# Performance work log

Hardware: AMD Instinct MI355X
Metric: run time of the kernel (lower is better)

Reference implementation:

```python
import jax, jax.numpy as jnp
import numpy as np

B, C_IN, H, W = 32, 3, 256, 256
PATCH = 16
E, C_OUT = 8, 8
C_PROJ = 16
NUM_CLASSES = 1000
SPP_LEVELS = (1, 2, 4)
GATE_STEEPNESS = 10.0


def _conv(x, w, b, pad):
    # x: [N,C,H,W], w: [O,C,kh,kw]
    y = jax.lax.conv_general_dilated(x, w, (1, 1), [(pad, pad), (pad, pad)],
                                     dimension_numbers=('NCHW', 'OIHW', 'NCHW'))
    return y + b[None, :, None, None]


def _forward(X, expert_w, expert_b, proj_w, proj_b, keys, threshold,
             final_w, final_b, lin_w, lin_b):
    Bx, C, Hx, Wx = X.shape
    h, w = Hx // PATCH, Wx // PATCH
    P = h * w
    # 1) patch extraction: [B,C,H,W] -> [B*P, C, ph, pw]
    xp = (X.reshape(Bx, C, h, PATCH, w, PATCH)
           .transpose(0, 2, 4, 1, 3, 5)
           .reshape(Bx * P, C, PATCH, PATCH))
    # 2) router: conv projection -> global avg pool -> key similarity -> softmax -> soft threshold gate
    proj = _conv(xp, proj_w, proj_b, 1)                 # [BP, 16, ph, pw]
    pooled = proj.mean(axis=(2, 3))                     # [BP, 16]
    scores = jax.nn.softmax(pooled @ keys.T, axis=-1)   # [BP, E]
    gate = scores * jax.nn.sigmoid((scores - threshold) * GATE_STEEPNESS)
    gate = gate / (gate.sum(axis=-1, keepdims=True) + 1e-9)
    gate = gate.reshape(Bx, P, E)
    # 3) all experts fused as one conv with E*C_OUT output channels (conv3x3 pad1 + ReLU)
    ew = expert_w.reshape(E * C_OUT, C, 3, 3)
    eb = expert_b.reshape(E * C_OUT)
    outs = jax.nn.relu(_conv(xp, ew, eb, 1))            # [BP, E*Cout, ph, pw]
    outs = outs.reshape(Bx, P, E, C_OUT, PATCH, PATCH)
    # 4) router-weighted combine over experts
    comb = jnp.einsum('bpe,bpeclm->bpclm', gate, outs)  # [B,P,Cout,ph,pw]
    # 5) reassemble patches -> [B, Cout, H, W]
    y = (comb.reshape(Bx, h, w, C_OUT, PATCH, PATCH)
             .transpose(0, 3, 1, 4, 2, 5)
             .reshape(Bx, C_OUT, h * PATCH, w * PATCH))
    # 6) final 1x1 conv with padding=4 (zero-pad input, bias added everywhere)
    ypad = jnp.pad(y, ((0, 0), (0, 0), (4, 4), (4, 4)))
    y = jnp.einsum('oc,bchw->bohw', final_w[:, :, 0, 0], ypad) + final_b[None, :, None, None]
    # 7) spatial pyramid pooling (levels 1,2,4) -> [B, Cout*21]
    Bc, Cc, Hc, Wc = y.shape
    feats = [y.reshape(Bc, Cc, l, Hc // l, l, Wc // l).mean(axis=(3, 5)).reshape(Bc, -1)
             for l in SPP_LEVELS]
    spp = jnp.concatenate(feats, axis=-1)
    # 8) classification head
    return spp @ lin_w + lin_b


def setup_inputs() -> dict:
    key = jax.random.key(0)
    ks = jax.random.split(key, 11)
    s = 0.1
    spp_dim = C_OUT * sum(l * l for l in SPP_LEVELS)  # 168
    return {
        'X': jax.random.normal(ks[0], (B, C_IN, H, W), jnp.float32),
        'expert_w': jax.random.normal(ks[1], (E, C_OUT, C_IN, 3, 3), jnp.float32) * s,
        'expert_b': jax.random.normal(ks[2], (E, C_OUT), jnp.float32) * s,
        'proj_w': jax.random.normal(ks[3], (C_PROJ, C_IN, 3, 3), jnp.float32) * s,
        'proj_b': jax.random.normal(ks[4], (C_PROJ,), jnp.float32) * s,
        'keys': jax.random.normal(ks[5], (E, C_PROJ), jnp.float32) * s,
        'threshold': jnp.array(0.125, jnp.float32),
        'final_w': jax.random.normal(ks[6], (C_OUT, C_OUT, 1, 1), jnp.float32) * s,
        'final_b': jax.random.normal(ks[7], (C_OUT,), jnp.float32) * s,
        'lin_w': jax.random.normal(ks[8], (spp_dim, NUM_CLASSES), jnp.float32) * s,
        'lin_b': jax.random.normal(ks[9], (NUM_CLASSES,), jnp.float32) * s,
    }


def reference(X, expert_w, expert_b, proj_w, proj_b, keys, threshold,
              final_w, final_b, lin_w, lin_b):
    return _forward(X, expert_w, expert_b, proj_w, proj_b, keys, threshold,
                    final_w, final_b, lin_w, lin_b)
```

## Files before the change

### kernel.cpp

```cpp
#include <hip/hip_runtime.h>
#include <hip/hip_bf16.h>
#include <math.h>


typedef short bf16x8 __attribute__((ext_vector_type(8)));
typedef float f32x4 __attribute__((ext_vector_type(4)));
typedef float pf2 __attribute__((ext_vector_type(2)));

__device__ __forceinline__ int cellOf(int r) {
    int rr = r + 4;
    return (rr >= 66) + (rr >= 132) + (rr >= 198);
}

__device__ __forceinline__ unsigned int packbf2(float lo, float hi) {
    __hip_bfloat162 h = __float22bfloat162_rn(make_float2(lo, hi));
    unsigned int u;
    __builtin_memcpy(&u, &h, 4);
    return u;
}

__global__ __launch_bounds__(256) void prep_kernel(
    const float* __restrict__ ew, const float* __restrict__ ebg,
    const float* __restrict__ pw, const float* __restrict__ pb,
    const float* __restrict__ keys, float* __restrict__ Sy,
    unsigned short* __restrict__ Bg, float* __restrict__ cbf)
{
    const int t = threadIdx.x;
    for (int i = t; i < 8192; i += 256) Sy[i] = 0.f;
    if (t < 72) {
        float sv[32];
        #pragma unroll
        for (int s = 0; s < 32; ++s) {
            int q, kx; bool zz = false;
            if (s < 16)       { q = s >> 1;  kx = s & 1; }
            else if (s < 18)  { q = 8;       kx = s - 16; }
            else if (s < 26)  { q = s - 18;  kx = 2; }
            else if (s == 26) { q = 8;       kx = 2; }
            else              { q = 0; kx = 0; zz = true; }
            const int ky = q / 3, c = q - ky * 3;
            const int widx = c * 9 + ky * 3 + kx;
            float a;
            if (t < 64) {
                a = ew[t * 27 + widx];
            } else {
                const int e = t - 64;
                a = 0.f;
                #pragma unroll
                for (int o = 0; o < 16; ++o)
                    a += keys[e * 16 + o] * pw[o * 27 + widx];
            }
            sv[s] = zz ? 0.f : a;
        }
        uint4 q0, q1, q2v, q3v;
        q0.x  = packbf2(sv[0],  sv[1]);  q0.y  = packbf2(sv[2],  sv[3]);
        q0.z  = packbf2(sv[4],  sv[5]);  q0.w  = packbf2(sv[6],  sv[7]);
        q1.x  = packbf2(sv[8],  sv[9]);  q1.y  = packbf2(sv[10], sv[11]);
        q1.z  = packbf2(sv[12], sv[13]); q1.w  = packbf2(sv[14], sv[15]);
        q2v.x = packbf2(sv[16], sv[17]); q2v.y = packbf2(sv[18], sv[19]);
        q2v.z = packbf2(sv[20], sv[21]); q2v.w = packbf2(sv[22], sv[23]);
        q3v.x = packbf2(sv[24], sv[25]); q3v.y = packbf2(sv[26], sv[27]);
        q3v.z = packbf2(sv[28], sv[29]); q3v.w = packbf2(sv[30], sv[31]);
        uint4* dst = reinterpret_cast<uint4*>(&Bg[t * 32]);
        dst[0] = q0; dst[1] = q1; dst[2] = q2v; dst[3] = q3v;
    }
    if (t >= 128 && t < 208) {
        const int i = t - 128;
        float c;
        if (i < 64) {
            c = ebg[i];
        } else {
            const int e = (i - 64) & 7;
            c = 0.f;
            #pragma unroll
            for (int o = 0; o < 16; ++o) c += keys[e * 16 + o] * pb[o];
        }
        cbf[i] = c;
    }
}

#define CONV_STEP(SB, ACCJ) do {                                            \
    uint4 pkv;                                                              \
    pkv.x = pkw[offp0 + (SB)];                                              \
    pkv.y = pkw[offp1 + (SB)];                                              \
    pkv.z = pkw[offp2 + (SB)];                                              \
    pkv.w = pkw[offp3 + (SB)];                                              \
    const bf16x8 afr = __builtin_bit_cast(bf16x8, pkv);                     \
    const f32x4 a0 = __builtin_amdgcn_mfma_f32_16x16x32_bf16(afr, bfr0, cbv0, 0, 0, 0); \
    const f32x4 a1 = __builtin_amdgcn_mfma_f32_16x16x32_bf16(afr, bfr1, cbv1, 0, 0, 0); \
    const f32x4 a2 = __builtin_amdgcn_mfma_f32_16x16x32_bf16(afr, bfr2, cbv2, 0, 0, 0); \
    const f32x4 a3 = __builtin_amdgcn_mfma_f32_16x16x32_bf16(afr, bfr3, cbv3, 0, 0, 0); \
    a4acc = __builtin_amdgcn_mfma_f32_16x16x32_bf16(afr, bfr4, a4acc, 0, 0, 0); \
    const pf2 z2_ = {0.f, 0.f};                                             \
    {                                                                       \
        const pf2 l_ = __builtin_elementwise_max((pf2)__builtin_shufflevector(a0, a0, 0, 1), z2_); \
        const pf2 h_ = __builtin_elementwise_max((pf2)__builtin_shufflevector(a0, a0, 2, 3), z2_); \
        pall2[0] += l_ + h_;                                                \
        if (ACCJ) psb2[0] += l_ * jm2lo + h_ * jm2hi;                       \
    }                                                                       \
    {                                                                       \
        const pf2 l_ = __builtin_elementwise_max((pf2)__builtin_shufflevector(a1, a1, 0, 1), z2_); \
        const pf2 h_ = __builtin_elementwise_max((pf2)__builtin_shufflevector(a1, a1, 2, 3), z2_); \
        pall2[1] += l_ + h_;                                                \
        if (ACCJ) psb2[1] += l_ * jm2lo + h_ * jm2hi;                       \
    }                                                                       \
    {                                                                       \
        const pf2 l_ = __builtin_elementwise_max((pf2)__builtin_shufflevector(a2, a2, 0, 1), z2_); \
        const pf2 h_ = __builtin_elementwise_max((pf2)__builtin_shufflevector(a2, a2, 2, 3), z2_); \
        pall2[2] += l_ + h_;                                                \
        if (ACCJ) psb2[2] += l_ * jm2lo + h_ * jm2hi;                       \
    }                                                                       \
    {                                                                       \
        const pf2 l_ = __builtin_elementwise_max((pf2)__builtin_shufflevector(a3, a3, 0, 1), z2_); \
        const pf2 h_ = __builtin_elementwise_max((pf2)__builtin_shufflevector(a3, a3, 2, 3), z2_); \
        pall2[3] += l_ + h_;                                                \
        if (ACCJ) psb2[3] += l_ * jm2lo + h_ * jm2hi;                       \
    }                                                                       \
} while (0)

#define GATES_FROM_RSUM()                                                   \
    rsum += __shfl_xor(rsum, 16);                                           \
    rsum += __shfl_xor(rsum, 32);                                           \
    float gv[4];                                                            \
    {                                                                       \
        float lg = rsum * (1.f / 256.f);                                    \
        float mx = fmaxf(lg, __shfl_xor(lg, 1));                            \
        mx = fmaxf(mx, __shfl_xor(mx, 2));                                  \
        mx = fmaxf(mx, __shfl_xor(mx, 4));                                  \
        float ex = __expf(lg - mx);                                         \
        float s = ex;                                                       \
        s += __shfl_xor(s, 1); s += __shfl_xor(s, 2); s += __shfl_xor(s, 4);\
        float sc = ex / s;                                                  \
        float g = sc / (1.f + __expf(-(sc - thr) * 10.f));                  \
        float gs = g;                                                       \
        gs += __shfl_xor(gs, 1); gs += __shfl_xor(gs, 2); gs += __shfl_xor(gs, 4); \
        float gn = g / (gs + 1e-9f);                                        \
        const int gb = (lid & 56);                                          \
        const int hb = (lid >> 3) & 1;                                      \
        gv[0] = __shfl(gn, gb | (0 + hb));                                  \
        gv[1] = __shfl(gn, gb | (2 + hb));                                  \
        gv[2] = __shfl(gn, gb | (4 + hb));                                  \
        gv[3] = __shfl(gn, gb | (6 + hb));                                  \
    }

__global__ __launch_bounds__(128, 4) void fused_kernel(
    const float* __restrict__ X, const unsigned short* __restrict__ Bg,
    const float* __restrict__ thr_p, const float* __restrict__ cbf,
    float* __restrict__ Sy)
{
    __shared__ __align__(16) unsigned int pk[2][1952];

    const int t = threadIdx.x;
    const int wid = t >> 6, lid = t & 63;
    const int r16 = lid & 15, kb = lid >> 4;

    const int wgid = blockIdx.x;
    const int virt = (wgid & 7) * 512 + (wgid >> 3);

    const int gp = (virt << 1) + wid;
    const int b = gp >> 8;
    const int pi = (gp >> 4) & 15, pj = gp & 15;
    const int rbase = pi << 4, cbase = pj << 4;

    unsigned int* pkw = pk[wid];
    const float thr = thr_p[0];

    const int lr = lid >> 2, lq = lid & 3;
    const float* xb = X + ((b * 3) << 16) + ((rbase + lr) << 8) + cbase + (lq << 2);
    const float4 xv0 = *reinterpret_cast<const float4*>(xb);
    const float4 xv1 = *reinterpret_cast<const float4*>(xb + 65536);
    const float4 xv2 = *reinterpret_cast<const float4*>(xb + 131072);

    const bf16x8 bfr0 = *reinterpret_cast<const bf16x8*>(&Bg[(r16) * 32 + (kb << 3)]);
    const bf16x8 bfr1 = *reinterpret_cast<const bf16x8*>(&Bg[(16 + r16) * 32 + (kb << 3)]);
    const bf16x8 bfr2 = *reinterpret_cast<const bf16x8*>(&Bg[(32 + r16) * 32 + (kb << 3)]);
    const bf16x8 bfr3 = *reinterpret_cast<const bf16x8*>(&Bg[(48 + r16) * 32 + (kb << 3)]);
    const bf16x8 bfr4 = *reinterpret_cast<const bf16x8*>(&Bg[(64 + (r16 & 7)) * 32 + (kb << 3)]);

    const float cbs0 = cbf[r16];
    const float cbs1 = cbf[16 + r16];
    const float cbs2 = cbf[32 + r16];
    const float cbs3 = cbf[48 + r16];
    const float cbs4 = cbf[64 + r16];

    if (lid < 54) {
        pkw[lid] = 0u;
        pkw[918 + lid] = 0u;
        pkw[976 + lid] = 0u;
        pkw[1894 + lid] = 0u;
    }
    if (lid < 48) {
        const int y3 = lid / 3;
        const int cp = lid - y3 * 3;
        pkw[976 + (y3 + 1) * 54 + cp * 18 + 16] = 0u;
    }
    __builtin_amdgcn_wave_barrier();

    float s0 = __shfl_up(xv0.w, 1);
    float s1 = __shfl_up(xv1.w, 1);
    float s2 = __shfl_up(xv2.w, 1);
    const float c0p = (lq == 0) ? 0.f : s0;
    const float c1p = (lq == 0) ? 0.f : s1;
    const float c2p = (lq == 0) ? 0.f : s2;
    float nxx = __shfl_down(xv0.x, 4);
    float nxy = __shfl_down(xv0.y, 4);
    float nxz = __shfl_down(xv0.z, 4);
    float nxw = __shfl_down(xv0.w, 4);
    if (lr == 15) { nxx = 0.f; nxy = 0.f; nxz = 0.f; nxw = 0.f; }

    {
        const int y = lr + 1;
        const int b2 = y * 54 + (lq << 2);
        unsigned int u0, u1, u2, u3;
        u0 = packbf2(c0p,   xv0.x); u1 = packbf2(xv0.x, xv0.y);
        u2 = packbf2(xv0.y, xv0.z); u3 = packbf2(xv0.z, xv0.w);
        *reinterpret_cast<uint2*>(&pkw[b2])      = make_uint2(u0, u1);
        *reinterpret_cast<uint2*>(&pkw[b2 + 2])  = make_uint2(u2, u3);
        u0 = packbf2(c1p,   xv1.x); u1 = packbf2(xv1.x, xv1.y);
        u2 = packbf2(xv1.y, xv1.z); u3 = packbf2(xv1.z, xv1.w);
        *reinterpret_cast<uint2*>(&pkw[b2 + 18]) = make_uint2(u0, u1);
        *reinterpret_cast<uint2*>(&pkw[b2 + 20]) = make_uint2(u2, u3);
        u0 = packbf2(c2p,   xv2.x); u1 = packbf2(xv2.x, xv2.y);
        u2 = packbf2(xv2.y, xv2.z); u3 = packbf2(xv2.z, xv2.w);
        *reinterpret_cast<uint2*>(&pkw[b2 + 36]) = make_uint2(u0, u1);
        *reinterpret_cast<uint2*>(&pkw[b2 + 38]) = make_uint2(u2, u3);

        const int bx = 976 + y * 54 + (lq << 2);
        u0 = packbf2(xv0.x, xv1.x); u1 = packbf2(xv0.y, xv1.y);
        u2 = packbf2(xv0.z, xv1.z); u3 = packbf2(xv0.w, xv1.w);
        *reinterpret_cast<uint2*>(&pkw[bx])      = make_uint2(u0, u1);
        *reinterpret_cast<uint2*>(&pkw[bx + 2])  = make_uint2(u2, u3);
        u0 = packbf2(xv1.x, xv2.x); u1 = packbf2(xv1.y, xv2.y);
        u2 = packbf2(xv1.z, xv2.z); u3 = packbf2(xv1.w, xv2.w);
        *reinterpret_cast<uint2*>(&pkw[bx + 18]) = make_uint2(u0, u1);
        *reinterpret_cast<uint2*>(&pkw[bx + 20]) = make_uint2(u2, u3);
        u0 = packbf2(xv2.x, nxx);  u1 = packbf2(xv2.y, nxy);
        u2 = packbf2(xv2.z, nxz);  u3 = packbf2(xv2.w, nxw);
        *reinterpret_cast<uint2*>(&pkw[bx + 36]) = make_uint2(u0, u1);
        *reinterpret_cast<uint2*>(&pkw[bx + 38]) = make_uint2(u2, u3);

        if (lr == 0) {
            const int b0 = 976 + 36 + (lq << 2);
            u0 = packbf2(0.f, xv0.x); u1 = packbf2(0.f, xv0.y);
            u2 = packbf2(0.f, xv0.z); u3 = packbf2(0.f, xv0.w);
            *reinterpret_cast<uint2*>(&pkw[b0])     = make_uint2(u0, u1);
            *reinterpret_cast<uint2*>(&pkw[b0 + 2]) = make_uint2(u2, u3);
        }
    }
    __builtin_amdgcn_wave_barrier();

    int offp0, offp1, offp2, offp3;
    if (kb < 2) {
        const int t0 = kb * 72 + r16;
        offp0 = t0; offp1 = t0 + 18; offp2 = t0 + 36; offp3 = t0 + 54;
    } else if (kb == 2) {
        offp0 = 144 + r16; offp1 = 977 + r16; offp2 = 1013 + r16; offp3 = 1049 + r16;
    } else {
        offp0 = 1085 + r16; offp1 = 1121 + r16; offp2 = 1121 + r16; offp3 = 1121 + r16;
    }

    const f32x4 cbv0 = {cbs0, cbs0, cbs0, cbs0};
    const f32x4 cbv1 = {cbs1, cbs1, cbs1, cbs1};
    const f32x4 cbv2 = {cbs2, cbs2, cbs2, cbs2};
    const f32x4 cbv3 = {cbs3, cbs3, cbs3, cbs3};
    const float rb16 = cbs4 * 16.f;
    f32x4 a4acc = {rb16, rb16, rb16, rb16};

    const int iA = cellOf(rbase), iB = cellOf(rbase + 15);
    const int jA = cellOf(cbase), jB = cellOf(cbase + 15);
    const int isp = (iA + 1) * 66 - 4 - rbase;
    const int jsp = (jA + 1) * 66 - 4 - cbase;
    const bool anySplit = (isp < 16) | (jsp < 16);

    const int bc16 = b << 4;
    const pf2 zz2 = {0.f, 0.f};

    if (!anySplit) {
        pf2 pall2[4] = {zz2, zz2, zz2, zz2};
        pf2 psb2[4]  = {zz2, zz2, zz2, zz2};
        pf2 jm2lo = zz2, jm2hi = zz2;
        #pragma unroll
        for (int mt = 0; mt < 16; ++mt) CONV_STEP(mt * 54, 0);

        float rsum = (a4acc[0] + a4acc[1]) + (a4acc[2] + a4acc[3]);
        GATES_FROM_RSUM();

        float tt = 0.f;
        #pragma unroll
        for (int nt = 0; nt < 4; ++nt)
            tt = fmaf(gv[nt], pall2[nt].x + pall2[nt].y, tt);
        tt += __shfl_xor(tt, 8);
        tt += __shfl_xor(tt, 16);
        tt += __shfl_xor(tt, 32);
        if (lid < 8)
            atomicAdd(&Sy[(iA * 4 + jA) * 512 + bc16 + lid], tt);
    } else {
        float jmask[4];
        #pragma unroll
        for (int r = 0; r < 4; ++r)
            jmask[r] = ((kb << 2) + r >= jsp) ? 1.f : 0.f;
        const pf2 jm2lo = {jmask[0], jmask[1]};
        const pf2 jm2hi = {jmask[2], jmask[3]};

        pf2 pall2[4] = {zz2, zz2, zz2, zz2};
        pf2 psb2[4]  = {zz2, zz2, zz2, zz2};
        const int m1 = isp < 16 ? isp : 16;

        int sb = 0;
        for (int mt = 0; mt < m1; ++mt) { CONV_STEP(sb, 1); sb += 54; }
        const float pa0_0 = pall2[0].x + pall2[0].y;
        const float pa0_1 = pall2[1].x + pall2[1].y;
        const float pa0_2 = pall2[2].x + pall2[2].y;
        const float pa0_3 = pall2[3].x + pall2[3].y;
        const float pb0_0 = psb2[0].x + psb2[0].y;
        const float pb0_1 = psb2[1].x + psb2[1].y;
        const float pb0_2 = psb2[2].x + psb2[2].y;
        const float pb0_3 = psb2[3].x + psb2[3].y;
        pall2[0] = pall2[1] = pall2[2] = pall2[3] = zz2;
        psb2[0] = psb2[1] = psb2[2] = psb2[3] = zz2;
        for (int mt = m1; mt < 16; ++mt) { CONV_STEP(sb, 1); sb += 54; }

        float rsum = (a4acc[0] + a4acc[1]) + (a4acc[2] + a4acc[3]);
        GATES_FROM_RSUM();

        float tTA = gv[0] * pa0_0 + gv[1] * pa0_1 + gv[2] * pa0_2 + gv[3] * pa0_3;
        float tTB = gv[0] * pb0_0 + gv[1] * pb0_1 + gv[2] * pb0_2 + gv[3] * pb0_3;
        float tBA = 0.f, tBB = 0.f;
        #pragma unroll
        for (int nt = 0; nt < 4; ++nt) {
            tBA = fmaf(gv[nt], pall2[nt].x + pall2[nt].y, tBA);
            tBB = fmaf(gv[nt], psb2[nt].x + psb2[nt].y, tBB);
        }
        #pragma unroll
        for (int m = 8; m <= 32; m <<= 1) {
            tTA += __shfl_xor(tTA, m);
            tTB += __shfl_xor(tTB, m);
            tBA += __shfl_xor(tBA, m);
            tBB += __shfl_xor(tBB, m);
        }
        if (lid < 8) {
            atomicAdd(&Sy[(iA * 4 + jA) * 512 + bc16 + lid], tTA - tTB);
            atomicAdd(&Sy[(iA * 4 + jB) * 512 + bc16 + lid], tTB);
            atomicAdd(&Sy[(iB * 4 + jA) * 512 + bc16 + lid], tBA - tBB);
            atomicAdd(&Sy[(iB * 4 + jB) * 512 + bc16 + lid], tBB);
        }
    }
}

__global__ __launch_bounds__(256) void head_kernel(
    const float* __restrict__ Sy, const float* __restrict__ fw,
    const float* __restrict__ fb, const float* __restrict__ lw,
    const float* __restrict__ lb, float* __restrict__ out)
{
    __shared__ float syl[128];
    __shared__ float s2[32];
    __shared__ float stot[8];
    __shared__ float spp[168];
    const int t = threadIdx.x;
    const int b = blockIdx.y;
    if (t < 128) syl[t] = Sy[(t & 15) * 512 + b * 16 + (t >> 4)];
    __syncthreads();
    if (t < 32) {
        int c = t >> 2, I = (t >> 1) & 1, J = t & 1;
        const float* p = &syl[c * 16];
        s2[t] = p[(2 * I) * 4 + 2 * J] + p[(2 * I) * 4 + 2 * J + 1] +
                p[(2 * I + 1) * 4 + 2 * J] + p[(2 * I + 1) * 4 + 2 * J + 1];
    } else if (t >= 32 && t < 40) {
        int c = t - 32;
        float s = 0.f;
        #pragma unroll
        for (int i2 = 0; i2 < 16; ++i2) s += syl[c * 16 + i2];
        stot[c] = s;
    }
    __syncthreads();
    if (t < 168) {
        float acc = 0.f;
        int o;
        if (t < 8) {
            o = t;
            #pragma unroll
            for (int c = 0; c < 8; ++c) acc += fw[o * 8 + c] * stot[c];
            acc *= (1.f / 69696.f);
        } else if (t < 40) {
            int m = t - 8; o = m >> 2; int q = m & 3;
            #pragma unroll
            for (int c = 0; c < 8; ++c) acc += fw[o * 8 + c] * s2[c * 4 + q];
            acc *= (1.f / 17424.f);
        } else {
            int m = t - 40; o = m >> 4; int cell = m & 15;
            #pragma unroll
            for (int c = 0; c < 8; ++c) acc += fw[o * 8 + c] * syl[c * 16 + cell];
            acc *= (1.f / 4356.f);
        }
        spp[t] = acc + fb[o];
    }
    __syncthreads();
    const int n = blockIdx.x * 256 + t;
    if (n < 1000) {
        float acc = lb[n];
        for (int k = 0; k < 168; ++k) acc = fmaf(spp[k], lw[k * 1000 + n], acc);
        out[b * 1000 + n] = acc;
    }
}

extern "C" void kernel_launch(void* const* d_in, const int* in_sizes, int n_in,
                              void* d_out, int out_size, void* d_ws, size_t ws_size,
                              hipStream_t stream) {
    const float* X    = (const float*)d_in[0];
    const float* ew   = (const float*)d_in[1];
    const float* eb   = (const float*)d_in[2];
    const float* pw   = (const float*)d_in[3];
    const float* pb   = (const float*)d_in[4];
    const float* keys = (const float*)d_in[5];
    const float* thr  = (const float*)d_in[6];
    const float* fw   = (const float*)d_in[7];
    const float* fb   = (const float*)d_in[8];
    const float* lw   = (const float*)d_in[9];
    const float* lb   = (const float*)d_in[10];
    float* out = (float*)d_out;
    float* Sy  = (float*)d_ws;
    unsigned short* Bg = (unsigned short*)((float*)d_ws + 8192);
    float* cbf = (float*)d_ws + 9344;

    prep_kernel<<<1, 256, 0, stream>>>(ew, eb, pw, pb, keys, Sy, Bg, cbf);
    fused_kernel<<<4096, 128, 0, stream>>>(X, Bg, thr, cbf, Sy);
    head_kernel<<<dim3(4, 32), 256, 0, stream>>>(Sy, fw, fb, lw, lb, out);
}
```

Baseline: 38.71 us.

## Process two patches per wave to share weight fragments and halve grid

Each wave now handles two patches (from different batches, judging by the bA/bB indices), packing two LDS slabs and interleaving MFMA chains for both. The weight and bias fragments loaded per wave are reused across two patches, and the grid shrinks from 4096 to 2048 workgroups. This amortises per-wave setup and gives the scheduler independent MFMA chains to overlap. In exchange it raises register and LDS use per wave, which can lower occupancy.

```diff
diff --git a/kernel.cpp b/kernel.cpp
--- a/kernel.cpp
+++ b/kernel.cpp
@@ -78,110 +78,7 @@
     }
 }
 
-#define CONV_STEP(SB, ACCJ) do {                                            \
-    uint4 pkv;                                                              \
-    pkv.x = pkw[offp0 + (SB)];                                              \
-    pkv.y = pkw[offp1 + (SB)];                                              \
-    pkv.z = pkw[offp2 + (SB)];                                              \
-    pkv.w = pkw[offp3 + (SB)];                                              \
-    const bf16x8 afr = __builtin_bit_cast(bf16x8, pkv);                     \
-    const f32x4 a0 = __builtin_amdgcn_mfma_f32_16x16x32_bf16(afr, bfr0, cbv0, 0, 0, 0); \
-    const f32x4 a1 = __builtin_amdgcn_mfma_f32_16x16x32_bf16(afr, bfr1, cbv1, 0, 0, 0); \
-    const f32x4 a2 = __builtin_amdgcn_mfma_f32_16x16x32_bf16(afr, bfr2, cbv2, 0, 0, 0); \
-    const f32x4 a3 = __builtin_amdgcn_mfma_f32_16x16x32_bf16(afr, bfr3, cbv3, 0, 0, 0); \
-    a4acc = __builtin_amdgcn_mfma_f32_16x16x32_bf16(afr, bfr4, a4acc, 0, 0, 0); \
-    const pf2 z2_ = {0.f, 0.f};                                             \
-    {                                                                       \
-        const pf2 l_ = __builtin_elementwise_max((pf2)__builtin_shufflevector(a0, a0, 0, 1), z2_); \
-        const pf2 h_ = __builtin_elementwise_max((pf2)__builtin_shufflevector(a0, a0, 2, 3), z2_); \
-        pall2[0] += l_ + h_;                                                \
-        if (ACCJ) psb2[0] += l_ * jm2lo + h_ * jm2hi;                       \
-    }                                                                       \
-    {                                                                       \
-        const pf2 l_ = __builtin_elementwise_max((pf2)__builtin_shufflevector(a1, a1, 0, 1), z2_); \
-        const pf2 h_ = __builtin_elementwise_max((pf2)__builtin_shufflevector(a1, a1, 2, 3), z2_); \
-        pall2[1] += l_ + h_;                                                \
-        if (ACCJ) psb2[1] += l_ * jm2lo + h_ * jm2hi;                       \
-    }                                                                       \
-    {                                                                       \
-        const pf2 l_ = __builtin_elementwise_max((pf2)__builtin_shufflevector(a2, a2, 0, 1), z2_); \
-        const pf2 h_ = __builtin_elementwise_max((pf2)__builtin_shufflevector(a2, a2, 2, 3), z2_); \
-        pall2[2] += l_ + h_;                                                \
-        if (ACCJ) psb2[2] += l_ * jm2lo + h_ * jm2hi;                       \
-    }                                                                       \
-    {                                                                       \
-        const pf2 l_ = __builtin_elementwise_max((pf2)__builtin_shufflevector(a3, a3, 0, 1), z2_); \
-        const pf2 h_ = __builtin_elementwise_max((pf2)__builtin_shufflevector(a3, a3, 2, 3), z2_); \
-        pall2[3] += l_ + h_;                                                \
-        if (ACCJ) psb2[3] += l_ * jm2lo + h_ * jm2hi;                       \
-    }                                                                       \
-} while (0)
-
-#define GATES_FROM_RSUM()                                                   \
-    rsum += __shfl_xor(rsum, 16);                                           \
-    rsum += __shfl_xor(rsum, 32);                                           \
-    float gv[4];                                                            \
-    {                                                                       \
-        float lg = rsum * (1.f / 256.f);                                    \
-        float mx = fmaxf(lg, __shfl_xor(lg, 1));                            \
-        mx = fmaxf(mx, __shfl_xor(mx, 2));                                  \
-        mx = fmaxf(mx, __shfl_xor(mx, 4));                                  \
-        float ex = __expf(lg - mx);                                         \
-        float s = ex;                                                       \
-        s += __shfl_xor(s, 1); s += __shfl_xor(s, 2); s += __shfl_xor(s, 4);\
-        float sc = ex / s;                                                  \
-        float g = sc / (1.f + __expf(-(sc - thr) * 10.f));                  \
-        float gs = g;                                                       \
-        gs += __shfl_xor(gs, 1); gs += __shfl_xor(gs, 2); gs += __shfl_xor(gs, 4); \
-        float gn = g / (gs + 1e-9f);                                        \
-        const int gb = (lid & 56);                                          \
-        const int hb = (lid >> 3) & 1;                                      \
-        gv[0] = __shfl(gn, gb | (0 + hb));                                  \
-        gv[1] = __shfl(gn, gb | (2 + hb));                                  \
-        gv[2] = __shfl(gn, gb | (4 + hb));                                  \
-        gv[3] = __shfl(gn, gb | (6 + hb));                                  \
-    }
-
-__global__ __launch_bounds__(128, 4) void fused_kernel(
-    const float* __restrict__ X, const unsigned short* __restrict__ Bg,
-    const float* __restrict__ thr_p, const float* __restrict__ cbf,
-    float* __restrict__ Sy)
-{
-    __shared__ __align__(16) unsigned int pk[2][1952];
-
-    const int t = threadIdx.x;
-    const int wid = t >> 6, lid = t & 63;
-    const int r16 = lid & 15, kb = lid >> 4;
-
-    const int wgid = blockIdx.x;
-    const int virt = (wgid & 7) * 512 + (wgid >> 3);
-
-    const int gp = (virt << 1) + wid;
-    const int b = gp >> 8;
-    const int pi = (gp >> 4) & 15, pj = gp & 15;
-    const int rbase = pi << 4, cbase = pj << 4;
-
-    unsigned int* pkw = pk[wid];
-    const float thr = thr_p[0];
-
-    const int lr = lid >> 2, lq = lid & 3;
-    const float* xb = X + ((b * 3) << 16) + ((rbase + lr) << 8) + cbase + (lq << 2);
-    const float4 xv0 = *reinterpret_cast<const float4*>(xb);
-    const float4 xv1 = *reinterpret_cast<const float4*>(xb + 65536);
-    const float4 xv2 = *reinterpret_cast<const float4*>(xb + 131072);
-
-    const bf16x8 bfr0 = *reinterpret_cast<const bf16x8*>(&Bg[(r16) * 32 + (kb << 3)]);
-    const bf16x8 bfr1 = *reinterpret_cast<const bf16x8*>(&Bg[(16 + r16) * 32 + (kb << 3)]);
-    const bf16x8 bfr2 = *reinterpret_cast<const bf16x8*>(&Bg[(32 + r16) * 32 + (kb << 3)]);
-    const bf16x8 bfr3 = *reinterpret_cast<const bf16x8*>(&Bg[(48 + r16) * 32 + (kb << 3)]);
-    const bf16x8 bfr4 = *reinterpret_cast<const bf16x8*>(&Bg[(64 + (r16 & 7)) * 32 + (kb << 3)]);
-
-    const float cbs0 = cbf[r16];
-    const float cbs1 = cbf[16 + r16];
-    const float cbs2 = cbf[32 + r16];
-    const float cbs3 = cbf[48 + r16];
-    const float cbs4 = cbf[64 + r16];
-
+__device__ __forceinline__ void zero_halo(unsigned int* pkw, const int lid) {
     if (lid < 54) {
         pkw[lid] = 0u;
         pkw[918 + lid] = 0u;
@@ -193,8 +90,11 @@
         const int cp = lid - y3 * 3;
         pkw[976 + (y3 + 1) * 54 + cp * 18 + 16] = 0u;
     }
-    __builtin_amdgcn_wave_barrier();
-
+}
+
+__device__ __forceinline__ void pack_slab(unsigned int* pkw, const int lr,
+                                          const int lq, const float4 xv0,
+                                          const float4 xv1, const float4 xv2) {
     float s0 = __shfl_up(xv0.w, 1);
     float s1 = __shfl_up(xv1.w, 1);
     float s2 = __shfl_up(xv2.w, 1);
@@ -207,45 +107,169 @@
     float nxw = __shfl_down(xv0.w, 4);
     if (lr == 15) { nxx = 0.f; nxy = 0.f; nxz = 0.f; nxw = 0.f; }
 
-    {
-        const int y = lr + 1;
-        const int b2 = y * 54 + (lq << 2);
-        unsigned int u0, u1, u2, u3;
-        u0 = packbf2(c0p,   xv0.x); u1 = packbf2(xv0.x, xv0.y);
-        u2 = packbf2(xv0.y, xv0.z); u3 = packbf2(xv0.z, xv0.w);
-        *reinterpret_cast<uint2*>(&pkw[b2])      = make_uint2(u0, u1);
-        *reinterpret_cast<uint2*>(&pkw[b2 + 2])  = make_uint2(u2, u3);
-        u0 = packbf2(c1p,   xv1.x); u1 = packbf2(xv1.x, xv1.y);
-        u2 = packbf2(xv1.y, xv1.z); u3 = packbf2(xv1.z, xv1.w);
-        *reinterpret_cast<uint2*>(&pkw[b2 + 18]) = make_uint2(u0, u1);
-        *reinterpret_cast<uint2*>(&pkw[b2 + 20]) = make_uint2(u2, u3);
-        u0 = packbf2(c2p,   xv2.x); u1 = packbf2(xv2.x, xv2.y);
-        u2 = packbf2(xv2.y, xv2.z); u3 = packbf2(xv2.z, xv2.w);
-        *reinterpret_cast<uint2*>(&pkw[b2 + 36]) = make_uint2(u0, u1);
-        *reinterpret_cast<uint2*>(&pkw[b2 + 38]) = make_uint2(u2, u3);
-
-        const int bx = 976 + y * 54 + (lq << 2);
-        u0 = packbf2(xv0.x, xv1.x); u1 = packbf2(xv0.y, xv1.y);
-        u2 = packbf2(xv0.z, xv1.z); u3 = packbf2(xv0.w, xv1.w);
-        *reinterpret_cast<uint2*>(&pkw[bx])      = make_uint2(u0, u1);
-        *reinterpret_cast<uint2*>(&pkw[bx + 2])  = make_uint2(u2, u3);
-        u0 = packbf2(xv1.x, xv2.x); u1 = packbf2(xv1.y, xv2.y);
-        u2 = packbf2(xv1.z, xv2.z); u3 = packbf2(xv1.w, xv2.w);
-        *reinterpret_cast<uint2*>(&pkw[bx + 18]) = make_uint2(u0, u1);
-        *reinterpret_cast<uint2*>(&pkw[bx + 20]) = make_uint2(u2, u3);
-        u0 = packbf2(xv2.x, nxx);  u1 = packbf2(xv2.y, nxy);
-        u2 = packbf2(xv2.z, nxz);  u3 = packbf2(xv2.w, nxw);
-        *reinterpret_cast<uint2*>(&pkw[bx + 36]) = make_uint2(u0, u1);
-        *reinterpret_cast<uint2*>(&pkw[bx + 38]) = make_uint2(u2, u3);
-
-        if (lr == 0) {
-            const int b0 = 976 + 36 + (lq << 2);
-            u0 = packbf2(0.f, xv0.x); u1 = packbf2(0.f, xv0.y);
-            u2 = packbf2(0.f, xv0.z); u3 = packbf2(0.f, xv0.w);
-            *reinterpret_cast<uint2*>(&pkw[b0])     = make_uint2(u0, u1);
-            *reinterpret_cast<uint2*>(&pkw[b0 + 2]) = make_uint2(u2, u3);
-        }
-    }
+    const int y = lr + 1;
+    const int b2 = y * 54 + (lq << 2);
+    unsigned int u0, u1, u2, u3;
+    u0 = packbf2(c0p,   xv0.x); u1 = packbf2(xv0.x, xv0.y);
+    u2 = packbf2(xv0.y, xv0.z); u3 = packbf2(xv0.z, xv0.w);
+    *reinterpret_cast<uint2*>(&pkw[b2])      = make_uint2(u0, u1);
+    *reinterpret_cast<uint2*>(&pkw[b2 + 2])  = make_uint2(u2, u3);
+    u0 = packbf2(c1p,   xv1.x); u1 = packbf2(xv1.x, xv1.y);
+    u2 = packbf2(xv1.y, xv1.z); u3 = packbf2(xv1.z, xv1.w);
+    *reinterpret_cast<uint2*>(&pkw[b2 + 18]) = make_uint2(u0, u1);
+    *reinterpret_cast<uint2*>(&pkw[b2 + 20]) = make_uint2(u2, u3);
+    u0 = packbf2(c2p,   xv2.x); u1 = packbf2(xv2.x, xv2.y);
+    u2 = packbf2(xv2.y, xv2.z); u3 = packbf2(xv2.z, xv2.w);
+    *reinterpret_cast<uint2*>(&pkw[b2 + 36]) = make_uint2(u0, u1);
+    *reinterpret_cast<uint2*>(&pkw[b2 + 38]) = make_uint2(u2, u3);
+
+    const int bx = 976 + y * 54 + (lq << 2);
+    u0 = packbf2(xv0.x, xv1.x); u1 = packbf2(xv0.y, xv1.y);
+    u2 = packbf2(xv0.z, xv1.z); u3 = packbf2(xv0.w, xv1.w);
+    *reinterpret_cast<uint2*>(&pkw[bx])      = make_uint2(u0, u1);
+    *reinterpret_cast<uint2*>(&pkw[bx + 2])  = make_uint2(u2, u3);
+    u0 = packbf2(xv1.x, xv2.x); u1 = packbf2(xv1.y, xv2.y);
+    u2 = packbf2(xv1.z, xv2.z); u3 = packbf2(xv1.w, xv2.w);
+    *reinterpret_cast<uint2*>(&pkw[bx + 18]) = make_uint2(u0, u1);
+    *reinterpret_cast<uint2*>(&pkw[bx + 20]) = make_uint2(u2, u3);
+    u0 = packbf2(xv2.x, nxx);  u1 = packbf2(xv2.y, nxy);
+    u2 = packbf2(xv2.z, nxz);  u3 = packbf2(xv2.w, nxw);
+    *reinterpret_cast<uint2*>(&pkw[bx + 36]) = make_uint2(u0, u1);
+    *reinterpret_cast<uint2*>(&pkw[bx + 38]) = make_uint2(u2, u3);
+
+    if (lr == 0) {
+        const int b0 = 976 + 36 + (lq << 2);
+        u0 = packbf2(0.f, xv0.x); u1 = packbf2(0.f, xv0.y);
+        u2 = packbf2(0.f, xv0.z); u3 = packbf2(0.f, xv0.w);
+        *reinterpret_cast<uint2*>(&pkw[b0])     = make_uint2(u0, u1);
+        *reinterpret_cast<uint2*>(&pkw[b0 + 2]) = make_uint2(u2, u3);
+    }
+}
+
+#define MFMA_ACC(AF, A4, PALL, PSB, ACCJ) do {                              \
+    const f32x4 a0_ = __builtin_amdgcn_mfma_f32_16x16x32_bf16(AF, bfr0, cbv0, 0, 0, 0); \
+    const f32x4 a1_ = __builtin_amdgcn_mfma_f32_16x16x32_bf16(AF, bfr1, cbv1, 0, 0, 0); \
+    const f32x4 a2_ = __builtin_amdgcn_mfma_f32_16x16x32_bf16(AF, bfr2, cbv2, 0, 0, 0); \
+    const f32x4 a3_ = __builtin_amdgcn_mfma_f32_16x16x32_bf16(AF, bfr3, cbv3, 0, 0, 0); \
+    A4 = __builtin_amdgcn_mfma_f32_16x16x32_bf16(AF, bfr4, A4, 0, 0, 0);    \
+    const pf2 z2_ = {0.f, 0.f};                                             \
+    {                                                                       \
+        const pf2 l_ = __builtin_elementwise_max((pf2)__builtin_shufflevector(a0_, a0_, 0, 1), z2_); \
+        const pf2 h_ = __builtin_elementwise_max((pf2)__builtin_shufflevector(a0_, a0_, 2, 3), z2_); \
+        PALL[0] += l_ + h_;                                                 \
+        if (ACCJ) PSB[0] += l_ * jm2lo + h_ * jm2hi;                        \
+    }                                                                       \
+    {                                                                       \
+        const pf2 l_ = __builtin_elementwise_max((pf2)__builtin_shufflevector(a1_, a1_, 0, 1), z2_); \
+        const pf2 h_ = __builtin_elementwise_max((pf2)__builtin_shufflevector(a1_, a1_, 2, 3), z2_); \
+        PALL[1] += l_ + h_;                                                 \
+        if (ACCJ) PSB[1] += l_ * jm2lo + h_ * jm2hi;                        \
+    }                                                                       \
+    {                                                                       \
+        const pf2 l_ = __builtin_elementwise_max((pf2)__builtin_shufflevector(a2_, a2_, 0, 1), z2_); \
+        const pf2 h_ = __builtin_elementwise_max((pf2)__builtin_shufflevector(a2_, a2_, 2, 3), z2_); \
+        PALL[2] += l_ + h_;                                                 \
+        if (ACCJ) PSB[2] += l_ * jm2lo + h_ * jm2hi;                        \
+    }                                                                       \
+    {                                                                       \
+        const pf2 l_ = __builtin_elementwise_max((pf2)__builtin_shufflevector(a3_, a3_, 0, 1), z2_); \
+        const pf2 h_ = __builtin_elementwise_max((pf2)__builtin_shufflevector(a3_, a3_, 2, 3), z2_); \
+        PALL[3] += l_ + h_;                                                 \
+        if (ACCJ) PSB[3] += l_ * jm2lo + h_ * jm2hi;                        \
+    }                                                                       \
+} while (0)
+
+#define CONV_STEP2(SB, ACCJ) do {                                           \
+    uint4 pkvA, pkvB;                                                       \
+    pkvA.x = pkwA[offp0 + (SB)];                                            \
+    pkvA.y = pkwA[offp1 + (SB)];                                            \
+    pkvA.z = pkwA[offp2 + (SB)];                                            \
+    pkvA.w = pkwA[offp3 + (SB)];                                            \
+    pkvB.x = pkwB[offp0 + (SB)];                                            \
+    pkvB.y = pkwB[offp1 + (SB)];                                            \
+    pkvB.z = pkwB[offp2 + (SB)];                                            \
+    pkvB.w = pkwB[offp3 + (SB)];                                            \
+    const bf16x8 afA = __builtin_bit_cast(bf16x8, pkvA);                    \
+    const bf16x8 afB = __builtin_bit_cast(bf16x8, pkvB);                    \
+    MFMA_ACC(afA, a4A, pallA, psbA, ACCJ);                                  \
+    MFMA_ACC(afB, a4B, pallB, psbB, ACCJ);                                  \
+} while (0)
+
+#define GATES_COMPUTE(RSUM, GV) do {                                        \
+    RSUM += __shfl_xor(RSUM, 16);                                           \
+    RSUM += __shfl_xor(RSUM, 32);                                           \
+    float lg = RSUM * (1.f / 256.f);                                        \
+    float mx = fmaxf(lg, __shfl_xor(lg, 1));                                \
+    mx = fmaxf(mx, __shfl_xor(mx, 2));                                      \
+    mx = fmaxf(mx, __shfl_xor(mx, 4));                                      \
+    float ex = __expf(lg - mx);                                             \
+    float s = ex;                                                           \
+    s += __shfl_xor(s, 1); s += __shfl_xor(s, 2); s += __shfl_xor(s, 4);    \
+    float sc = ex / s;                                                      \
+    float g = sc / (1.f + __expf(-(sc - thr) * 10.f));                      \
+    float gs = g;                                                           \
+    gs += __shfl_xor(gs, 1); gs += __shfl_xor(gs, 2); gs += __shfl_xor(gs, 4); \
+    float gn = g / (gs + 1e-9f);                                            \
+    const int gb_ = (lid & 56);                                             \
+    const int hb_ = (lid >> 3) & 1;                                         \
+    GV[0] = __shfl(gn, gb_ | (0 + hb_));                                    \
+    GV[1] = __shfl(gn, gb_ | (2 + hb_));                                    \
+    GV[2] = __shfl(gn, gb_ | (4 + hb_));                                    \
+    GV[3] = __shfl(gn, gb_ | (6 + hb_));                                    \
+} while (0)
+
+__global__ __launch_bounds__(128, 2) void fused_kernel(
+    const float* __restrict__ X, const unsigned short* __restrict__ Bg,
+    const float* __restrict__ thr_p, const float* __restrict__ cbf,
+    float* __restrict__ Sy)
+{
+    __shared__ __align__(16) unsigned int pk[2][2][1952];
+
+    const int t = threadIdx.x;
+    const int wid = t >> 6, lid = t & 63;
+    const int r16 = lid & 15, kb = lid >> 4;
+
+    const int wgid = blockIdx.x;
+    const int virt = (wgid & 7) * 256 + (wgid >> 3);
+    const int q = (virt << 1) | wid;
+
+    const int bA = q >> 8;
+    const int bB = bA + 16;
+    const int pi = (q >> 4) & 15, pj = q & 15;
+    const int rbase = pi << 4, cbase = pj << 4;
+
+    unsigned int* pkwA = pk[wid][0];
+    unsigned int* pkwB = pk[wid][1];
+    const float thr = thr_p[0];
+
+    const int lr = lid >> 2, lq = lid & 3;
+    const float* xbA = X + ((bA * 3) << 16) + ((rbase + lr) << 8) + cbase + (lq << 2);
+    const float* xbB = xbA + (48 << 16);
+    const float4 a0v = *reinterpret_cast<const float4*>(xbA);
+    const float4 a1v = *reinterpret_cast<const float4*>(xbA + 65536);
+    const float4 a2v = *reinterpret_cast<const float4*>(xbA + 131072);
+    const float4 b0v = *reinterpret_cast<const float4*>(xbB);
+    const float4 b1v = *reinterpret_cast<const float4*>(xbB + 65536);
+    const float4 b2v = *reinterpret_cast<const float4*>(xbB + 131072);
+
+    const bf16x8 bfr0 = *reinterpret_cast<const bf16x8*>(&Bg[(r16) * 32 + (kb << 3)]);
+    const bf16x8 bfr1 = *reinterpret_cast<const bf16x8*>(&Bg[(16 + r16) * 32 + (kb << 3)]);
+    const bf16x8 bfr2 = *reinterpret_cast<const bf16x8*>(&Bg[(32 + r16) * 32 + (kb << 3)]);
+    const bf16x8 bfr3 = *reinterpret_cast<const bf16x8*>(&Bg[(48 + r16) * 32 + (kb << 3)]);
+    const bf16x8 bfr4 = *reinterpret_cast<const bf16x8*>(&Bg[(64 + (r16 & 7)) * 32 + (kb << 3)]);
+
+    const float cbs0 = cbf[r16];
+    const float cbs1 = cbf[16 + r16];
+    const float cbs2 = cbf[32 + r16];
+    const float cbs3 = cbf[48 + r16];
+    const float cbs4 = cbf[64 + r16];
+
+    zero_halo(pkwA, lid);
+    zero_halo(pkwB, lid);
+    __builtin_amdgcn_wave_barrier();
+
+    pack_slab(pkwA, lr, lq, a0v, a1v, a2v);
+    pack_slab(pkwB, lr, lq, b0v, b1v, b2v);
     __builtin_amdgcn_wave_barrier();
 
     int offp0, offp1, offp2, offp3;
@@ -263,7 +287,8 @@
     const f32x4 cbv2 = {cbs2, cbs2, cbs2, cbs2};
     const f32x4 cbv3 = {cbs3, cbs3, cbs3, cbs3};
     const float rb16 = cbs4 * 16.f;
-    f32x4 a4acc = {rb16, rb16, rb16, rb16};
+    f32x4 a4A = {rb16, rb16, rb16, rb16};
+    f32x4 a4B = {rb16, rb16, rb16, rb16};
 
     const int iA = cellOf(rbase), iB = cellOf(rbase + 15);
     const int jA = cellOf(cbase), jB = cellOf(cbase + 15);
@@ -271,28 +296,38 @@
     const int jsp = (jA + 1) * 66 - 4 - cbase;
     const bool anySplit = (isp < 16) | (jsp < 16);
 
-    const int bc16 = b << 4;
     const pf2 zz2 = {0.f, 0.f};
 
     if (!anySplit) {
-        pf2 pall2[4] = {zz2, zz2, zz2, zz2};
-        pf2 psb2[4]  = {zz2, zz2, zz2, zz2};
+        pf2 pallA[4] = {zz2, zz2, zz2, zz2};
+        pf2 pallB[4] = {zz2, zz2, zz2, zz2};
+        pf2 psbA[4], psbB[4];
         pf2 jm2lo = zz2, jm2hi = zz2;
-        #pragma unroll
-        for (int mt = 0; mt < 16; ++mt) CONV_STEP(mt * 54, 0);
-
-        float rsum = (a4acc[0] + a4acc[1]) + (a4acc[2] + a4acc[3]);
-        GATES_FROM_RSUM();
-
-        float tt = 0.f;
-        #pragma unroll
-        for (int nt = 0; nt < 4; ++nt)
-            tt = fmaf(gv[nt], pall2[nt].x + pall2[nt].y, tt);
-        tt += __shfl_xor(tt, 8);
-        tt += __shfl_xor(tt, 16);
-        tt += __shfl_xor(tt, 32);
-        if (lid < 8)
-            atomicAdd(&Sy[(iA * 4 + jA) * 512 + bc16 + lid], tt);
+        (void)psbA; (void)psbB; (void)jm2lo; (void)jm2hi;
+        #pragma unroll
+        for (int mt = 0; mt < 16; ++mt) CONV_STEP2(mt * 54, 0);
+
+        float rsA = (a4A[0] + a4A[1]) + (a4A[2] + a4A[3]);
+        float rsB = (a4B[0] + a4B[1]) + (a4B[2] + a4B[3]);
+        float gvA[4], gvB[4];
+        GATES_COMPUTE(rsA, gvA);
+        GATES_COMPUTE(rsB, gvB);
+
+        float ttA = 0.f, ttB = 0.f;
+        #pragma unroll
+        for (int nt = 0; nt < 4; ++nt) {
+            ttA = fmaf(gvA[nt], pallA[nt].x + pallA[nt].y, ttA);
+            ttB = fmaf(gvB[nt], pallB[nt].x + pallB[nt].y, ttB);
+        }
+        #pragma unroll
+        for (int m = 8; m <= 32; m <<= 1) {
+            ttA += __shfl_xor(ttA, m);
+            ttB += __shfl_xor(ttB, m);
+        }
+        if (lid < 8) {
+            atomicAdd(&Sy[(iA * 4 + jA) * 512 + (bA << 4) + lid], ttA);
+            atomicAdd(&Sy[(iA * 4 + jA) * 512 + (bB << 4) + lid], ttB);
+        }
     } else {
         float jmask[4];
         #pragma unroll
@@ -301,47 +336,77 @@
         const pf2 jm2lo = {jmask[0], jmask[1]};
         const pf2 jm2hi = {jmask[2], jmask[3]};
 
-        pf2 pall2[4] = {zz2, zz2, zz2, zz2};
-        pf2 psb2[4]  = {zz2, zz2, zz2, zz2};
+        pf2 pallA[4] = {zz2, zz2, zz2, zz2};
+        pf2 psbA[4]  = {zz2, zz2, zz2, zz2};
+        pf2 pallB[4] = {zz2, zz2, zz2, zz2};
+        pf2 psbB[4]  = {zz2, zz2, zz2, zz2};
         const int m1 = isp < 16 ? isp : 16;
 
         int sb = 0;
-        for (int mt = 0; mt < m1; ++mt) { CONV_STEP(sb, 1); sb += 54; }
-        const float pa0_0 = pall2[0].x + pall2[0].y;
-        const float pa0_1 = pall2[1].x + pall2[1].y;
-        const float pa0_2 = pall2[2].x + pall2[2].y;
-        const float pa0_3 = pall2[3].x + pall2[3].y;
-        const float pb0_0 = psb2[0].x + psb2[0].y;
-        const float pb0_1 = psb2[1].x + psb2[1].y;
-        const float pb0_2 = psb2[2].x + psb2[2].y;
-        const float pb0_3 = psb2[3].x + psb2[3].y;
-        pall2[0] = pall2[1] = pall2[2] = pall2[3] = zz2;
-        psb2[0] = psb2[1] = psb2[2] = psb2[3] = zz2;
-        for (int mt = m1; mt < 16; ++mt) { CONV_STEP(sb, 1); sb += 54; }
-
-        float rsum = (a4acc[0] + a4acc[1]) + (a4acc[2] + a4acc[3]);
-        GATES_FROM_RSUM();
-
-        float tTA = gv[0] * pa0_0 + gv[1] * pa0_1 + gv[2] * pa0_2 + gv[3] * pa0_3;
-        float tTB = gv[0] * pb0_0 + gv[1] * pb0_1 + gv[2] * pb0_2 + gv[3] * pb0_3;
-        float tBA = 0.f, tBB = 0.f;
+        for (int mt = 0; mt < m1; ++mt) { CONV_STEP2(sb, 1); sb += 54; }
+        const float paA0 = pallA[0].x + pallA[0].y;
+        const float paA1 = pallA[1].x + pallA[1].y;
+        const float paA2 = pallA[2].x + pallA[2].y;
+        const float paA3 = pallA[3].x + pallA[3].y;
+        const float pbA0 = psbA[0].x + psbA[0].y;
+        const float pbA1 = psbA[1].x + psbA[1].y;
+        const float pbA2 = psbA[2].x + psbA[2].y;
+        const float pbA3 = psbA[3].x + psbA[3].y;
+        const float paB0 = pallB[0].x + pallB[0].y;
+        const float paB1 = pallB[1].x + pallB[1].y;
+        const float paB2 = pallB[2].x + pallB[2].y;
+        const float paB3 = pallB[3].x + pallB[3].y;
+        const float pbB0 = psbB[0].x + psbB[0].y;
+        const float pbB1 = psbB[1].x + psbB[1].y;
+        const float pbB2 = psbB[2].x + psbB[2].y;
+        const float pbB3 = psbB[3].x + psbB[3].y;
+        pallA[0] = pallA[1] = pallA[2] = pallA[3] = zz2;
+        psbA[0] = psbA[1] = psbA[2] = psbA[3] = zz2;
+        pallB[0] = pallB[1] = pallB[2] = pallB[3] = zz2;
+        psbB[0] = psbB[1] = psbB[2] = psbB[3] = zz2;
+        for (int mt = m1; mt < 16; ++mt) { CONV_STEP2(sb, 1); sb += 54; }
+
+        float rsA = (a4A[0] + a4A[1]) + (a4A[2] + a4A[3]);
+        float rsB = (a4B[0] + a4B[1]) + (a4B[2] + a4B[3]);
+        float gvA[4], gvB[4];
+        GATES_COMPUTE(rsA, gvA);
+        GATES_COMPUTE(rsB, gvB);
+
+        float tTAa = gvA[0] * paA0 + gvA[1] * paA1 + gvA[2] * paA2 + gvA[3] * paA3;
+        float tTBa = gvA[0] * pbA0 + gvA[1] * pbA1 + gvA[2] * pbA2 + gvA[3] * pbA3;
+        float tTAb = gvB[0] * paB0 + gvB[1] * paB1 + gvB[2] * paB2 + gvB[3] * paB3;
+        float tTBb = gvB[0] * pbB0 + gvB[1] * pbB1 + gvB[2] * pbB2 + gvB[3] * pbB3;
+        float tBAa = 0.f, tBBa = 0.f, tBAb = 0.f, tBBb = 0.f;
         #pragma unroll
         for (int nt = 0; nt < 4; ++nt) {
-            tBA = fmaf(gv[nt], pall2[nt].x + pall2[nt].y, tBA);
-            tBB = fmaf(gv[nt], psb2[nt].x + psb2[nt].y, tBB);
+            tBAa = fmaf(gvA[nt], pallA[nt].x + pallA[nt].y, tBAa);
+            tBBa = fmaf(gvA[nt], psbA[nt].x + psbA[nt].y, tBBa);
+            tBAb = fmaf(gvB[nt], pallB[nt].x + pallB[nt].y, tBAb);
+            tBBb = fmaf(gvB[nt], psbB[nt].x + psbB[nt].y, tBBb);
         }
         #pragma unroll
         for (int m = 8; m <= 32; m <<= 1) {
-            tTA += __shfl_xor(tTA, m);
-            tTB += __shfl_xor(tTB, m);
-            tBA += __shfl_xor(tBA, m);
-            tBB += __shfl_xor(tBB, m);
+            tTAa += __shfl_xor(tTAa, m);
+            tTBa += __shfl_xor(tTBa, m);
+            tBAa += __shfl_xor(tBAa, m);
+            tBBa += __shfl_xor(tBBa, m);
+            tTAb += __shfl_xor(tTAb, m);
+            tTBb += __shfl_xor(tTBb, m);
+            tBAb += __shfl_xor(tBAb, m);
+            tBBb += __shfl_xor(tBBb, m);
         }
         if (lid < 8) {
-            atomicAdd(&Sy[(iA * 4 + jA) * 512 + bc16 + lid], tTA - tTB);
-            atomicAdd(&Sy[(iA * 4 + jB) * 512 + bc16 + lid], tTB);
-            atomicAdd(&Sy[(iB * 4 + jA) * 512 + bc16 + lid], tBA - tBB);
-            atomicAdd(&Sy[(iB * 4 + jB) * 512 + bc16 + lid], tBB);
+            const int cAA = (iA * 4 + jA) * 512, cAB = (iA * 4 + jB) * 512;
+            const int cBA = (iB * 4 + jA) * 512, cBB = (iB * 4 + jB) * 512;
+            const int oA = (bA << 4) + lid, oB = (bB << 4) + lid;
+            atomicAdd(&Sy[cAA + oA], tTAa - tTBa);
+            atomicAdd(&Sy[cAB + oA], tTBa);
+            atomicAdd(&Sy[cBA + oA], tBAa - tBBa);
+            atomicAdd(&Sy[cBB + oA], tBBa);
+            atomicAdd(&Sy[cAA + oB], tTAb - tTBb);
+            atomicAdd(&Sy[cAB + oB], tTBb);
+            atomicAdd(&Sy[cBA + oB], tBAb - tBBb);
+            atomicAdd(&Sy[cBB + oB], tBBb);
         }
     }
 }
@@ -422,6 +487,6 @@
     float* cbf = (float*)d_ws + 9344;
 
     prep_kernel<<<1, 256, 0, stream>>>(ew, eb, pw, pb, keys, Sy, Bg, cbf);
-    fused_kernel<<<4096, 128, 0, stream>>>(X, Bg, thr, cbf, Sy);
+    fused_kernel<<<2048, 128, 0, stream>>>(X, Bg, thr, cbf, Sy);
     head_kernel<<<dim3(4, 32), 256, 0, stream>>>(Sy, fw, fb, lw, lb, out);
 }
```

Result: slower. 43.12 us (+11.4%).
